# Optimization experiments

Measured on AMD Instinct MI355X. Metric: run time of the kernel, lower is better.

## Reference

```python
import jax, jax.numpy as jnp
import numpy as np

N, E, C = 8192, 8192, 256
AVG_DEG = 32


def _linear(x, w, b):
    return x @ w + b


def setup_inputs() -> dict:
    key = jax.random.key(0)
    ks = jax.random.split(key, 20)
    s = 1.0 / np.sqrt(C)
    x = jax.random.normal(ks[0], (N, C), dtype=jnp.float32)
    # binary adjacency with avg degree ~32 (unweighted COO -> dense 0/1 rep)
    adj = (jax.random.uniform(ks[1], (N, N)) < (AVG_DEG / N)).astype(jnp.float32)
    tar_ei = jax.random.randint(ks[2], (2, E), 0, N, dtype=jnp.int32)
    p = {
        'xlin_w1': jax.random.uniform(ks[3], (C, C), minval=-s, maxval=s),
        'xlin_b1': jnp.zeros((C,), jnp.float32),
        'xlin_w2': jax.random.uniform(ks[4], (C, C), minval=-s, maxval=s),
        'xlin_b2': jnp.zeros((C,), jnp.float32),
        'xcn_w1': jax.random.uniform(ks[5], (C, C), minval=-s, maxval=s),
        'xcn_b1': jnp.zeros((C,), jnp.float32),
        'xcn_w2': jax.random.uniform(ks[6], (C, C), minval=-s, maxval=s),
        'xcn_b2': jnp.zeros((C,), jnp.float32),
        'xij_w': jax.random.uniform(ks[7], (C, C), minval=-s, maxval=s),
        'xij_b': jnp.zeros((C,), jnp.float32),
        'lin_w1': jax.random.uniform(ks[8], (C, C), minval=-s, maxval=s),
        'lin_b1': jnp.zeros((C,), jnp.float32),
        'lin_w2': jax.random.uniform(ks[9], (C, 1), minval=-s, maxval=s),
        'lin_b2': jnp.zeros((1,), jnp.float32),
        'beta': jnp.ones((1,), jnp.float32),
    }
    return {'x': x, 'adj': adj, 'tar_ei': tar_ei, **p}


def reference(x, adj, tar_ei,
              xlin_w1, xlin_b1, xlin_w2, xlin_b2,
              xcn_w1, xcn_b1, xcn_w2, xcn_b2,
              xij_w, xij_b,
              lin_w1, lin_b1, lin_w2, lin_b2, beta):
    i, j = tar_ei[0], tar_ei[1]
    xi = x[i]                      # [E, C]
    xj = x[j]                      # [E, C]
    # x = x + xlin(x): Linear-ReLU-Linear-ReLU (dropout inactive, ln=Identity)
    h = x + jax.nn.relu(_linear(jax.nn.relu(_linear(x, xlin_w1, xlin_b1)), xlin_w2, xlin_b2))
    # adjoverlap: common-neighbor mask per target edge, cn[e,k] = A[i_e,k]*A[j_e,k]
    cn = adj[i] * adj[j]           # [E, N]
    # spmm_add(cn, h)
    xcn = cn @ h                   # [E, C]
    # xijlin: Linear-ReLU (tailact -> Identity tail)
    xij = jax.nn.relu(_linear(xi * xj, xij_w, xij_b))
    # xcnlin: Linear-ReLU-Linear-ReLU
    xcn = jax.nn.relu(_linear(jax.nn.relu(_linear(xcn, xcn_w1, xcn_b1)), xcn_w2, xcn_b2))
    # lin: Linear-ReLU-Linear(out)
    z = xcn * beta + xij
    out = _linear(jax.nn.relu(_linear(z, lin_w1, lin_b1)), lin_w2, lin_b2)
    return out  # [E, 1]
```

## Files before the change

### kernel.cpp

```cpp
#include <hip/hip_runtime.h>
#include <cstdint>
#include <cstddef>


#define C_DIM   256
#define N_NODES 8192
#define E_EDGES 8192

typedef short bf16x8 __attribute__((ext_vector_type(8)));
typedef float f32x4  __attribute__((ext_vector_type(4)));

struct WPtrs { const float* p[6]; };

__device__ __forceinline__ unsigned short bf16_rne(float a) {
    unsigned u = __float_as_uint(a);
    u += 0x7FFFu + ((u >> 16) & 1u);
    return (unsigned short)(u >> 16);
}
__device__ __forceinline__ void split2(float v, short& h, short& l) {
    unsigned short hb = bf16_rne(v);
    h = (short)hb;
    l = (short)bf16_rne(v - __uint_as_float((unsigned)hb << 16));
}

__global__ __launch_bounds__(256) void k_prep(const float* __restrict__ adj,
                                              unsigned long long* __restrict__ bits,
                                              WPtrs wp, short* __restrict__ WFH,
                                              short* __restrict__ WFL) {
    const int t = threadIdx.x;
    if (blockIdx.x < 48) {
        __shared__ float tile[32][257];
        const int g  = blockIdx.x >> 3;
        const int kf = blockIdx.x & 7;
        const float* W = wp.p[g];
        #pragma unroll
        for (int p = 0; p < 8; ++p) {
            int s = t + (p << 8);
            int row = s >> 6, c4 = s & 63;
            float4 v = *(const float4*)&W[(size_t)(kf * 32 + row) * C_DIM + (c4 << 2)];
            tile[row][(c4 << 2) + 0] = v.x; tile[row][(c4 << 2) + 1] = v.y;
            tile[row][(c4 << 2) + 2] = v.z; tile[row][(c4 << 2) + 3] = v.w;
        }
        __syncthreads();
        #pragma unroll
        for (int p = 0; p < 4; ++p) {
            int s = t + (p << 8);
            int nf = s >> 6, lane = s & 63;
            int q = lane >> 4, fr = lane & 15;
            short h[8], l[8];
            #pragma unroll
            for (int e = 0; e < 8; ++e)
                split2(tile[q * 8 + e][nf * 16 + fr], h[e], l[e]);
            int dst = (g << 16) + (((kf * 16 + nf) << 6) + lane) * 8;
            *(short4*)&WFH[dst]     = make_short4(h[0], h[1], h[2], h[3]);
            *(short4*)&WFH[dst + 4] = make_short4(h[4], h[5], h[6], h[7]);
            *(short4*)&WFL[dst]     = make_short4(l[0], l[1], l[2], l[3]);
            *(short4*)&WFL[dst + 4] = make_short4(l[4], l[5], l[6], l[7]);
        }
    } else {
        const int TOTALW = N_NODES * N_NODES / 64;
        const int gw   = ((int)blockIdx.x - 48) * 4 + (t >> 6);
        const int lane = t & 63;
        const int NW   = 2048 * 4;
        for (int w = gw << 3; w < TOTALW; w += NW << 3) {
            float v[8];
            #pragma unroll
            for (int r = 0; r < 8; ++r)
                v[r] = adj[((size_t)(w + r) << 6) + lane];
            unsigned long long m[8];
            #pragma unroll
            for (int r = 0; r < 8; ++r)
                m[r] = __ballot(v[r] > 0.5f);
            if (lane == 0) {
                #pragma unroll
                for (int r = 0; r < 4; ++r) {
                    ulonglong2 u2; u2.x = m[2 * r]; u2.y = m[2 * r + 1];
                    *(ulonglong2*)&bits[w + 2 * r] = u2;
                }
            }
        }
    }
}

template<int MODE>
__device__ __forceinline__ void layer_sb(
    const short (*INH)[C_DIM], const short (*INL)[C_DIM],
    const short* __restrict__ WH, const short* __restrict__ WL,
    const float* __restrict__ bias,
    short (*POH)[C_DIM], short (*POL)[C_DIM], float (*FO)[C_DIM],
    float beta, const float* __restrict__ w2, float* __restrict__ out32)
{
    const int t = threadIdx.x, lane = t & 63, wq = t >> 6;
    const int fr = lane & 15, q = lane >> 4;
    f32x4 acc[2];
    #pragma unroll
    for (int i = 0; i < 2; ++i)
        #pragma unroll
        for (int r = 0; r < 4; ++r) acc[i][r] = 0.f;

    #pragma unroll 2
    for (int kf = 0; kf < 8; ++kf) {
        bf16x8 aH[2], aL[2];
        #pragma unroll
        for (int mf = 0; mf < 2; ++mf) {
            const int row = mf * 16 + fr;
            const int cc = (((kf << 2) + q) ^ (row & 7)) << 3;
            aH[mf] = *(const bf16x8*)&INH[row][cc];
            aL[mf] = *(const bf16x8*)&INL[row][cc];
        }
        const int wo = (((kf << 4) + wq) * 64 + lane) * 8;
        bf16x8 bH = *(const bf16x8*)&WH[wo];
        bf16x8 bL = *(const bf16x8*)&WL[wo];
        #pragma unroll
        for (int mf = 0; mf < 2; ++mf) {
            acc[mf] = __builtin_amdgcn_mfma_f32_16x16x32_bf16(aH[mf], bH, acc[mf], 0, 0, 0);
            acc[mf] = __builtin_amdgcn_mfma_f32_16x16x32_bf16(aH[mf], bL, acc[mf], 0, 0, 0);
            acc[mf] = __builtin_amdgcn_mfma_f32_16x16x32_bf16(aL[mf], bH, acc[mf], 0, 0, 0);
        }
    }

    const int col = (wq << 4) + fr;
    const float bb = bias[col];
    float gs[2][4];
    if (MODE == 4) {
        #pragma unroll
        for (int mf = 0; mf < 2; ++mf)
            #pragma unroll
            for (int r = 0; r < 4; ++r) gs[mf][r] = 0.f;
    }
    const float w2c = (MODE == 4) ? w2[col] : 0.f;
    #pragma unroll
    for (int mf = 0; mf < 2; ++mf)
        #pragma unroll
        for (int r = 0; r < 4; ++r) {
            const int row = mf * 16 + q * 4 + r;
            float v = fmaxf(acc[mf][r] + bb, 0.f);
            if (MODE == 0 || MODE == 1) {
                if (MODE == 1) v = v * beta + FO[row][col];
                short h, l;
                split2(v, h, l);
                const int cw = (((col >> 3) ^ (row & 7)) << 3) + (col & 7);
                POH[row][cw] = h;
                POL[row][cw] = l;
            } else if (MODE == 2) {
                FO[row][col] = v;
            } else {
                gs[mf][r] += v * w2c;
            }
        }
    if (MODE == 4) {
        #pragma unroll
        for (int mf = 0; mf < 2; ++mf)
            #pragma unroll
            for (int r = 0; r < 4; ++r) {
                float s = gs[mf][r];
                s += __shfl_xor(s, 1); s += __shfl_xor(s, 2);
                s += __shfl_xor(s, 4); s += __shfl_xor(s, 8);
                if (fr == 0) atomicAdd(&out32[mf * 16 + q * 4 + r], s);
            }
    }
}

__device__ __forceinline__ void layer_h2(
    const short (*INH)[C_DIM], const short (*INL)[C_DIM],
    const short* __restrict__ WH, const short* __restrict__ WL,
    const float* __restrict__ bias, const int* __restrict__ inst, int nrows,
    const float* __restrict__ xsrc, float (*XCN)[C_DIM])
{
    const int t = threadIdx.x, lane = t & 63, wq = t >> 6;
    const int fr = lane & 15, q = lane >> 4;
    f32x4 acc[2];
    #pragma unroll
    for (int i = 0; i < 2; ++i)
        #pragma unroll
        for (int r = 0; r < 4; ++r) acc[i][r] = 0.f;

    #pragma unroll 2
    for (int kf = 0; kf < 8; ++kf) {
        bf16x8 aH[2], aL[2];
        #pragma unroll
        for (int mf = 0; mf < 2; ++mf) {
            const int row = mf * 16 + fr;
            const int cc = (((kf << 2) + q) ^ (row & 7)) << 3;
            aH[mf] = *(const bf16x8*)&INH[row][cc];
            aL[mf] = *(const bf16x8*)&INL[row][cc];
        }
        const int wo = (((kf << 4) + wq) * 64 + lane) * 8;
        bf16x8 bH = *(const bf16x8*)&WH[wo];
        bf16x8 bL = *(const bf16x8*)&WL[wo];
        #pragma unroll
        for (int mf = 0; mf < 2; ++mf) {
            acc[mf] = __builtin_amdgcn_mfma_f32_16x16x32_bf16(aH[mf], bH, acc[mf], 0, 0, 0);
            acc[mf] = __builtin_amdgcn_mfma_f32_16x16x32_bf16(aH[mf], bL, acc[mf], 0, 0, 0);
            acc[mf] = __builtin_amdgcn_mfma_f32_16x16x32_bf16(aL[mf], bH, acc[mf], 0, 0, 0);
        }
    }
    const int col = (wq << 4) + fr;
    const float bb = bias[col];
    #pragma unroll
    for (int mf = 0; mf < 2; ++mf)
        #pragma unroll
        for (int r = 0; r < 4; ++r) {
            const int row = mf * 16 + q * 4 + r;
            if (row < nrows) {
                const int pk = inst[row];
                const int e  = pk >> 16;
                const int k  = pk & 0xffff;
                float v = fmaxf(acc[mf][r] + bb, 0.f) + xsrc[(size_t)k * C_DIM + col];
                atomicAdd(&XCN[e][col], v);
            }
        }
}

__global__ __launch_bounds__(1024, 1) void k_edge_mega(
    const unsigned long long* __restrict__ bits, const float* __restrict__ x,
    const int* __restrict__ tar,
    const short* __restrict__ WFH, const short* __restrict__ WFL,
    const float* __restrict__ b1x, const float* __restrict__ b2x,
    const float* __restrict__ bxij, const float* __restrict__ bcn1,
    const float* __restrict__ bcn2, const float* __restrict__ blin1,
    const float* __restrict__ betap, const float* __restrict__ w2,
    const float* __restrict__ b2o, float* __restrict__ out)
{
    __shared__ short AH[32][C_DIM], AL[32][C_DIM];
    __shared__ short BH[32][C_DIM], BL[32][C_DIM];
    __shared__ float CF[32][C_DIM];
    __shared__ int   eij2[32][2];
    __shared__ int   inst[1024];
    __shared__ int   cntot;
    __shared__ float out32[32];
    const int e0 = blockIdx.x << 5;
    const int t = threadIdx.x;
    if (t < 32) {
        eij2[t][0] = tar[e0 + t];
        eij2[t][1] = tar[E_EDGES + e0 + t];
        out32[t] = 0.f;
    }
    if (t == 0) cntot = 0;
    __syncthreads();
    #pragma unroll
    for (int p = 0; p < 8; ++p) {
        int idx = (p << 10) + t;
        CF[idx >> 8][idx & 255] = 0.f;
    }
    {
        const int le = t >> 5, sub = t & 31;
        const size_t bi = (size_t)eij2[le][0] * 128;
        const size_t bj = (size_t)eij2[le][1] * 128;
        #pragma unroll
        for (int w4 = 0; w4 < 4; ++w4) {
            const int w = (sub << 2) + w4;
            unsigned long long m = bits[bi + w] & bits[bj + w];
            while (m) {
                int b = __builtin_ctzll(m);
                int slot = atomicAdd(&cntot, 1);
                if (slot < 1024) inst[slot] = (le << 16) | ((w << 6) + b);
                m &= m - 1;
            }
        }
    }
    __syncthreads();
    const int ctot = min(cntot, 1024);
    for (int c0 = 0; c0 < ctot; c0 += 32) {
        const int nrows = min(32, ctot - c0);
        #pragma unroll
        for (int p = 0; p < 8; ++p) {
            int idx = (p << 10) + t;
            int r = idx >> 8, c = idx & 255;
            float v = 0.f;
            if (r < nrows) {
                int k = inst[c0 + r] & 0xffff;
                v = x[(size_t)k * C_DIM + c];
            }
            short h, l;
            split2(v, h, l);
            int cw = (((c >> 3) ^ (r & 7)) << 3) + (c & 7);
            AH[r][cw] = h;
            AL[r][cw] = l;
        }
        __syncthreads();
        layer_sb<0>(AH, AL, WFH + 0 * 65536, WFL + 0 * 65536, b1x,
                    BH, BL, nullptr, 0.f, nullptr, nullptr);
        __syncthreads();
        layer_h2(BH, BL, WFH + 1 * 65536, WFL + 1 * 65536, b2x,
                 inst + c0, nrows, x, CF);
        __syncthreads();
    }
    #pragma unroll
    for (int p = 0; p < 8; ++p) {
        int idx = (p << 10) + t;
        int r = idx >> 8, c = idx & 255;
        short h, l;
        split2(CF[r][c], h, l);
        int cw = (((c >> 3) ^ (r & 7)) << 3) + (c & 7);
        BH[r][cw] = h;
        BL[r][cw] = l;
    }
    __syncthreads();
    #pragma unroll
    for (int p = 0; p < 8; ++p) {
        int idx = (p << 10) + t;
        int e = idx >> 8, c = idx & 255;
        float v = x[(size_t)eij2[e][0] * C_DIM + c] * x[(size_t)eij2[e][1] * C_DIM + c];
        short h, l;
        split2(v, h, l);
        int cw = (((c >> 3) ^ (e & 7)) << 3) + (c & 7);
        AH[e][cw] = h;
        AL[e][cw] = l;
    }
    __syncthreads();
    const float beta = betap[0];
    layer_sb<2>(AH, AL, WFH + 2 * 65536, WFL + 2 * 65536, bxij,
                nullptr, nullptr, CF, 0.f, nullptr, nullptr);
    __syncthreads();
    layer_sb<0>(BH, BL, WFH + 3 * 65536, WFL + 3 * 65536, bcn1,
                AH, AL, nullptr, 0.f, nullptr, nullptr);
    __syncthreads();
    layer_sb<1>(AH, AL, WFH + 4 * 65536, WFL + 4 * 65536, bcn2,
                BH, BL, CF, beta, nullptr, nullptr);
    __syncthreads();
    layer_sb<4>(BH, BL, WFH + 5 * 65536, WFL + 5 * 65536, blin1,
                nullptr, nullptr, nullptr, 0.f, w2, out32);
    __syncthreads();
    if (t < 32) out[e0 + t] = out32[t] + b2o[0];
}

extern "C" void kernel_launch(void* const* d_in, const int* in_sizes, int n_in,
                              void* d_out, int out_size, void* d_ws, size_t ws_size,
                              hipStream_t stream) {
    const float* x       = (const float*)d_in[0];
    const float* adj     = (const float*)d_in[1];
    const int*   tar_ei  = (const int*)  d_in[2];
    const float* xlin_w1 = (const float*)d_in[3];
    const float* xlin_b1 = (const float*)d_in[4];
    const float* xlin_w2 = (const float*)d_in[5];
    const float* xlin_b2 = (const float*)d_in[6];
    const float* xcn_w1  = (const float*)d_in[7];
    const float* xcn_b1  = (const float*)d_in[8];
    const float* xcn_w2  = (const float*)d_in[9];
    const float* xcn_b2  = (const float*)d_in[10];
    const float* xij_w   = (const float*)d_in[11];
    const float* xij_b   = (const float*)d_in[12];
    const float* lin_w1  = (const float*)d_in[13];
    const float* lin_b1  = (const float*)d_in[14];
    const float* lin_w2  = (const float*)d_in[15];
    const float* lin_b2  = (const float*)d_in[16];
    const float* beta    = (const float*)d_in[17];
    float* out = (float*)d_out;

    char* ws = (char*)d_ws;
    const size_t MB = 1024 * 1024;
    unsigned long long* bits = (unsigned long long*)(ws);
    short* WFH  = (short*)(ws +  8 * MB);
    short* WFL  = (short*)(ws +  9 * MB);

    WPtrs wp;
    wp.p[0] = xlin_w1; wp.p[1] = xlin_w2; wp.p[2] = xij_w;
    wp.p[3] = xcn_w1;  wp.p[4] = xcn_w2;  wp.p[5] = lin_w1;

    hipLaunchKernelGGL(k_prep, dim3(48 + 2048), dim3(256), 0, stream,
                       adj, bits, wp, WFH, WFL);
    hipLaunchKernelGGL(k_edge_mega, dim3(E_EDGES / 32), dim3(1024), 0, stream,
                       bits, x, tar_ei, WFH, WFL,
                       xlin_b1, xlin_b2, xij_b, xcn_b1, xcn_b2, lin_b1,
                       beta, lin_w2, lin_b2, out);
}
```

Baseline: 85.58 us.

## Move xij branch GEMM into prep kernel to overlap with adjacency bitpacking

The xi*xj gather and xij linear+ReLU layer are moved out of the edge megakernel into 256 extra blocks of the prep kernel. These blocks run alongside the memory-bound adjacency bit-packing and write fp32 results to a workspace buffer. The megakernel then reads them from global memory in the MODE 1 epilogue, which shortens its serial chain of layers. In exchange the prep blocks split weights to bf16 on the fly from strided global loads, and an extra 8 MB fp32 round trip through global memory is added.

```diff
diff --git a/kernel.cpp b/kernel.cpp
--- a/kernel.cpp
+++ b/kernel.cpp
@@ -24,9 +24,13 @@
 }
 
 __global__ __launch_bounds__(256) void k_prep(const float* __restrict__ adj,
+                                              const float* __restrict__ x,
+                                              const int* __restrict__ tar,
                                               unsigned long long* __restrict__ bits,
                                               WPtrs wp, short* __restrict__ WFH,
-                                              short* __restrict__ WFL) {
+                                              short* __restrict__ WFL,
+                                              const float* __restrict__ bxij,
+                                              float* __restrict__ XIJF) {
     const int t = threadIdx.x;
     if (blockIdx.x < 48) {
         __shared__ float tile[32][257];
@@ -57,9 +61,89 @@
             *(short4*)&WFL[dst]     = make_short4(l[0], l[1], l[2], l[3]);
             *(short4*)&WFL[dst + 4] = make_short4(l[4], l[5], l[6], l[7]);
         }
+    } else if (blockIdx.x < 304) {
+        __shared__ short XH[32][C_DIM], XL[32][C_DIM];
+        __shared__ int   eij2[32][2];
+        const int e0 = ((int)blockIdx.x - 48) << 5;
+        if (t < 32) {
+            eij2[t][0] = tar[e0 + t];
+            eij2[t][1] = tar[E_EDGES + e0 + t];
+        }
+        __syncthreads();
+        #pragma unroll
+        for (int p = 0; p < 4; ++p) {
+            int idx = (p << 8) + t;
+            int r = idx >> 5, c = (idx & 31) << 3;
+            float4 a0 = *(const float4*)&x[(size_t)eij2[r][0] * C_DIM + c];
+            float4 a1 = *(const float4*)&x[(size_t)eij2[r][0] * C_DIM + c + 4];
+            float4 b0 = *(const float4*)&x[(size_t)eij2[r][1] * C_DIM + c];
+            float4 b1 = *(const float4*)&x[(size_t)eij2[r][1] * C_DIM + c + 4];
+            float v[8] = {a0.x * b0.x, a0.y * b0.y, a0.z * b0.z, a0.w * b0.w,
+                          a1.x * b1.x, a1.y * b1.y, a1.z * b1.z, a1.w * b1.w};
+            short h[8], l[8];
+            #pragma unroll
+            for (int e = 0; e < 8; ++e) split2(v[e], h[e], l[e]);
+            int cw = (((c >> 3) ^ (r & 7)) << 3);
+            *(short4*)&XH[r][cw]     = make_short4(h[0], h[1], h[2], h[3]);
+            *(short4*)&XH[r][cw + 4] = make_short4(h[4], h[5], h[6], h[7]);
+            *(short4*)&XL[r][cw]     = make_short4(l[0], l[1], l[2], l[3]);
+            *(short4*)&XL[r][cw + 4] = make_short4(l[4], l[5], l[6], l[7]);
+        }
+        __syncthreads();
+        const int lane = t & 63, w = t >> 6;
+        const int fr = lane & 15, q = lane >> 4;
+        const float* Wg = wp.p[2];
+        f32x4 acc[2][4];
+        #pragma unroll
+        for (int mf = 0; mf < 2; ++mf)
+            #pragma unroll
+            for (int nfi = 0; nfi < 4; ++nfi)
+                #pragma unroll
+                for (int r = 0; r < 4; ++r) acc[mf][nfi][r] = 0.f;
+        for (int kf = 0; kf < 8; ++kf) {
+            bf16x8 aH[2], aL[2];
+            #pragma unroll
+            for (int mf = 0; mf < 2; ++mf) {
+                const int row = mf * 16 + fr;
+                const int cc = (((kf << 2) + q) ^ (row & 7)) << 3;
+                aH[mf] = *(const bf16x8*)&XH[row][cc];
+                aL[mf] = *(const bf16x8*)&XL[row][cc];
+            }
+            #pragma unroll
+            for (int nfi = 0; nfi < 4; ++nfi) {
+                const int nf = (w << 2) + nfi;
+                bf16x8 bH, bL;
+                #pragma unroll
+                for (int e = 0; e < 8; ++e) {
+                    float wv = Wg[(size_t)(kf * 32 + q * 8 + e) * C_DIM + (nf << 4) + fr];
+                    short h, l;
+                    split2(wv, h, l);
+                    bH[e] = h; bL[e] = l;
+                }
+                #pragma unroll
+                for (int mf = 0; mf < 2; ++mf) {
+                    acc[mf][nfi] = __builtin_amdgcn_mfma_f32_16x16x32_bf16(aH[mf], bH, acc[mf][nfi], 0, 0, 0);
+                    acc[mf][nfi] = __builtin_amdgcn_mfma_f32_16x16x32_bf16(aH[mf], bL, acc[mf][nfi], 0, 0, 0);
+                    acc[mf][nfi] = __builtin_amdgcn_mfma_f32_16x16x32_bf16(aL[mf], bH, acc[mf][nfi], 0, 0, 0);
+                }
+            }
+        }
+        #pragma unroll
+        for (int nfi = 0; nfi < 4; ++nfi) {
+            const int col = ((w << 2) + nfi) * 16 + fr;
+            const float bb = bxij[col];
+            #pragma unroll
+            for (int mf = 0; mf < 2; ++mf)
+                #pragma unroll
+                for (int r = 0; r < 4; ++r) {
+                    const int row = mf * 16 + q * 4 + r;
+                    XIJF[(size_t)(e0 + row) * C_DIM + col] =
+                        fmaxf(acc[mf][nfi][r] + bb, 0.f);
+                }
+        }
     } else {
         const int TOTALW = N_NODES * N_NODES / 64;
-        const int gw   = ((int)blockIdx.x - 48) * 4 + (t >> 6);
+        const int gw   = ((int)blockIdx.x - 304) * 4 + (t >> 6);
         const int lane = t & 63;
         const int NW   = 2048 * 4;
         for (int w = gw << 3; w < TOTALW; w += NW << 3) {
@@ -87,7 +171,8 @@
     const short (*INH)[C_DIM], const short (*INL)[C_DIM],
     const short* __restrict__ WH, const short* __restrict__ WL,
     const float* __restrict__ bias,
-    short (*POH)[C_DIM], short (*POL)[C_DIM], float (*FO)[C_DIM],
+    short (*POH)[C_DIM], short (*POL)[C_DIM],
+    const float* __restrict__ xijg, int e0,
     float beta, const float* __restrict__ w2, float* __restrict__ out32)
 {
     const int t = threadIdx.x, lane = t & 63, wq = t >> 6;
@@ -136,14 +221,12 @@
             const int row = mf * 16 + q * 4 + r;
             float v = fmaxf(acc[mf][r] + bb, 0.f);
             if (MODE == 0 || MODE == 1) {
-                if (MODE == 1) v = v * beta + FO[row][col];
+                if (MODE == 1) v = v * beta + xijg[(size_t)(e0 + row) * C_DIM + col];
                 short h, l;
                 split2(v, h, l);
                 const int cw = (((col >> 3) ^ (row & 7)) << 3) + (col & 7);
                 POH[row][cw] = h;
                 POL[row][cw] = l;
-            } else if (MODE == 2) {
-                FO[row][col] = v;
             } else {
                 gs[mf][r] += v * w2c;
             }
@@ -217,9 +300,9 @@
     const int* __restrict__ tar,
     const short* __restrict__ WFH, const short* __restrict__ WFL,
     const float* __restrict__ b1x, const float* __restrict__ b2x,
-    const float* __restrict__ bxij, const float* __restrict__ bcn1,
-    const float* __restrict__ bcn2, const float* __restrict__ blin1,
-    const float* __restrict__ betap, const float* __restrict__ w2,
+    const float* __restrict__ bcn1, const float* __restrict__ bcn2,
+    const float* __restrict__ blin1, const float* __restrict__ betap,
+    const float* __restrict__ xijg, const float* __restrict__ w2,
     const float* __restrict__ b2o, float* __restrict__ out)
 {
     __shared__ short AH[32][C_DIM], AL[32][C_DIM];
@@ -280,7 +363,7 @@
         }
         __syncthreads();
         layer_sb<0>(AH, AL, WFH + 0 * 65536, WFL + 0 * 65536, b1x,
-                    BH, BL, nullptr, 0.f, nullptr, nullptr);
+                    BH, BL, nullptr, 0, 0.f, nullptr, nullptr);
         __syncthreads();
         layer_h2(BH, BL, WFH + 1 * 65536, WFL + 1 * 65536, b2x,
                  inst + c0, nrows, x, CF);
@@ -297,30 +380,15 @@
         BL[r][cw] = l;
     }
     __syncthreads();
-    #pragma unroll
-    for (int p = 0; p < 8; ++p) {
-        int idx = (p << 10) + t;
-        int e = idx >> 8, c = idx & 255;
-        float v = x[(size_t)eij2[e][0] * C_DIM + c] * x[(size_t)eij2[e][1] * C_DIM + c];
-        short h, l;
-        split2(v, h, l);
-        int cw = (((c >> 3) ^ (e & 7)) << 3) + (c & 7);
-        AH[e][cw] = h;
-        AL[e][cw] = l;
-    }
-    __syncthreads();
     const float beta = betap[0];
-    layer_sb<2>(AH, AL, WFH + 2 * 65536, WFL + 2 * 65536, bxij,
-                nullptr, nullptr, CF, 0.f, nullptr, nullptr);
-    __syncthreads();
     layer_sb<0>(BH, BL, WFH + 3 * 65536, WFL + 3 * 65536, bcn1,
-                AH, AL, nullptr, 0.f, nullptr, nullptr);
+                AH, AL, nullptr, 0, 0.f, nullptr, nullptr);
     __syncthreads();
     layer_sb<1>(AH, AL, WFH + 4 * 65536, WFL + 4 * 65536, bcn2,
-                BH, BL, CF, beta, nullptr, nullptr);
+                BH, BL, xijg, e0, beta, nullptr, nullptr);
     __syncthreads();
     layer_sb<4>(BH, BL, WFH + 5 * 65536, WFL + 5 * 65536, blin1,
-                nullptr, nullptr, nullptr, 0.f, w2, out32);
+                nullptr, nullptr, nullptr, 0, 0.f, w2, out32);
     __syncthreads();
     if (t < 32) out[e0 + t] = out32[t] + b2o[0];
 }
@@ -353,15 +421,16 @@
     unsigned long long* bits = (unsigned long long*)(ws);
     short* WFH  = (short*)(ws +  8 * MB);
     short* WFL  = (short*)(ws +  9 * MB);
+    float* XIJF = (float*)(ws + 10 * MB);
 
     WPtrs wp;
     wp.p[0] = xlin_w1; wp.p[1] = xlin_w2; wp.p[2] = xij_w;
     wp.p[3] = xcn_w1;  wp.p[4] = xcn_w2;  wp.p[5] = lin_w1;
 
-    hipLaunchKernelGGL(k_prep, dim3(48 + 2048), dim3(256), 0, stream,
-                       adj, bits, wp, WFH, WFL);
+    hipLaunchKernelGGL(k_prep, dim3(48 + 256 + 2048), dim3(256), 0, stream,
+                       adj, x, tar_ei, bits, wp, WFH, WFL, xij_b, XIJF);
     hipLaunchKernelGGL(k_edge_mega, dim3(E_EDGES / 32), dim3(1024), 0, stream,
                        bits, x, tar_ei, WFH, WFL,
-                       xlin_b1, xlin_b2, xij_b, xcn_b1, xcn_b2, lin_b1,
-                       beta, lin_w2, lin_b2, out);
-}
+                       xlin_b1, xlin_b2, xcn_b1, xcn_b2, lin_b1,
+                       beta, XIJF, lin_w2, lin_b2, out);
+}
```

Result: slower. 107.5 us (+25.6%).

## Replace shared-memory xcn atomics with register accumulation and hoist xij layer

Applied to the files above, without the earlier changes.

The float CF shared buffer and its per-element LDS atomicAdd scatter are removed. The second xlin layer now writes its rows as split bf16 into shared memory, and each thread scans the chunk's instance list to accumulate its edge's 8 columns in registers. The xij product and its linear layer are moved to the start of the kernel and kept in registers, so the LDS round trip for xij and a separate staging pass go away. The cost is a serial loop over the instances of each chunk in every thread and extra live registers across the main loop. Rounding also changes because the summed values are stored as hi/lo bf16 pairs before accumulation.

```diff
diff --git a/kernel.cpp b/kernel.cpp
--- a/kernel.cpp
+++ b/kernel.cpp
@@ -21,6 +21,9 @@
     unsigned short hb = bf16_rne(v);
     h = (short)hb;
     l = (short)bf16_rne(v - __uint_as_float((unsigned)hb << 16));
+}
+__device__ __forceinline__ float bf2f(short h) {
+    return __uint_as_float(((unsigned)(unsigned short)h) << 16);
 }
 
 __global__ __launch_bounds__(256) void k_prep(const float* __restrict__ adj,
@@ -82,22 +85,17 @@
     }
 }
 
-template<int MODE>
-__device__ __forceinline__ void layer_sb(
+__device__ __forceinline__ void layer_core(
     const short (*INH)[C_DIM], const short (*INL)[C_DIM],
     const short* __restrict__ WH, const short* __restrict__ WL,
-    const float* __restrict__ bias,
-    short (*POH)[C_DIM], short (*POL)[C_DIM], float (*FO)[C_DIM],
-    float beta, const float* __restrict__ w2, float* __restrict__ out32)
+    f32x4 acc[2])
 {
     const int t = threadIdx.x, lane = t & 63, wq = t >> 6;
     const int fr = lane & 15, q = lane >> 4;
-    f32x4 acc[2];
     #pragma unroll
     for (int i = 0; i < 2; ++i)
         #pragma unroll
         for (int r = 0; r < 4; ++r) acc[i][r] = 0.f;
-
     #pragma unroll 2
     for (int kf = 0; kf < 8; ++kf) {
         bf16x8 aH[2], aL[2];
@@ -118,98 +116,6 @@
             acc[mf] = __builtin_amdgcn_mfma_f32_16x16x32_bf16(aL[mf], bH, acc[mf], 0, 0, 0);
         }
     }
-
-    const int col = (wq << 4) + fr;
-    const float bb = bias[col];
-    float gs[2][4];
-    if (MODE == 4) {
-        #pragma unroll
-        for (int mf = 0; mf < 2; ++mf)
-            #pragma unroll
-            for (int r = 0; r < 4; ++r) gs[mf][r] = 0.f;
-    }
-    const float w2c = (MODE == 4) ? w2[col] : 0.f;
-    #pragma unroll
-    for (int mf = 0; mf < 2; ++mf)
-        #pragma unroll
-        for (int r = 0; r < 4; ++r) {
-            const int row = mf * 16 + q * 4 + r;
-            float v = fmaxf(acc[mf][r] + bb, 0.f);
-            if (MODE == 0 || MODE == 1) {
-                if (MODE == 1) v = v * beta + FO[row][col];
-                short h, l;
-                split2(v, h, l);
-                const int cw = (((col >> 3) ^ (row & 7)) << 3) + (col & 7);
-                POH[row][cw] = h;
-                POL[row][cw] = l;
-            } else if (MODE == 2) {
-                FO[row][col] = v;
-            } else {
-                gs[mf][r] += v * w2c;
-            }
-        }
-    if (MODE == 4) {
-        #pragma unroll
-        for (int mf = 0; mf < 2; ++mf)
-            #pragma unroll
-            for (int r = 0; r < 4; ++r) {
-                float s = gs[mf][r];
-                s += __shfl_xor(s, 1); s += __shfl_xor(s, 2);
-                s += __shfl_xor(s, 4); s += __shfl_xor(s, 8);
-                if (fr == 0) atomicAdd(&out32[mf * 16 + q * 4 + r], s);
-            }
-    }
-}
-
-__device__ __forceinline__ void layer_h2(
-    const short (*INH)[C_DIM], const short (*INL)[C_DIM],
-    const short* __restrict__ WH, const short* __restrict__ WL,
-    const float* __restrict__ bias, const int* __restrict__ inst, int nrows,
-    const float* __restrict__ xsrc, float (*XCN)[C_DIM])
-{
-    const int t = threadIdx.x, lane = t & 63, wq = t >> 6;
-    const int fr = lane & 15, q = lane >> 4;
-    f32x4 acc[2];
-    #pragma unroll
-    for (int i = 0; i < 2; ++i)
-        #pragma unroll
-        for (int r = 0; r < 4; ++r) acc[i][r] = 0.f;
-
-    #pragma unroll 2
-    for (int kf = 0; kf < 8; ++kf) {
-        bf16x8 aH[2], aL[2];
-        #pragma unroll
-        for (int mf = 0; mf < 2; ++mf) {
-            const int row = mf * 16 + fr;
-            const int cc = (((kf << 2) + q) ^ (row & 7)) << 3;
-            aH[mf] = *(const bf16x8*)&INH[row][cc];
-            aL[mf] = *(const bf16x8*)&INL[row][cc];
-        }
-        const int wo = (((kf << 4) + wq) * 64 + lane) * 8;
-        bf16x8 bH = *(const bf16x8*)&WH[wo];
-        bf16x8 bL = *(const bf16x8*)&WL[wo];
-        #pragma unroll
-        for (int mf = 0; mf < 2; ++mf) {
-            acc[mf] = __builtin_amdgcn_mfma_f32_16x16x32_bf16(aH[mf], bH, acc[mf], 0, 0, 0);
-            acc[mf] = __builtin_amdgcn_mfma_f32_16x16x32_bf16(aH[mf], bL, acc[mf], 0, 0, 0);
-            acc[mf] = __builtin_amdgcn_mfma_f32_16x16x32_bf16(aL[mf], bH, acc[mf], 0, 0, 0);
-        }
-    }
-    const int col = (wq << 4) + fr;
-    const float bb = bias[col];
-    #pragma unroll
-    for (int mf = 0; mf < 2; ++mf)
-        #pragma unroll
-        for (int r = 0; r < 4; ++r) {
-            const int row = mf * 16 + q * 4 + r;
-            if (row < nrows) {
-                const int pk = inst[row];
-                const int e  = pk >> 16;
-                const int k  = pk & 0xffff;
-                float v = fmaxf(acc[mf][r] + bb, 0.f) + xsrc[(size_t)k * C_DIM + col];
-                atomicAdd(&XCN[e][col], v);
-            }
-        }
 }
 
 __global__ __launch_bounds__(1024, 1) void k_edge_mega(
@@ -224,13 +130,17 @@
 {
     __shared__ short AH[32][C_DIM], AL[32][C_DIM];
     __shared__ short BH[32][C_DIM], BL[32][C_DIM];
-    __shared__ float CF[32][C_DIM];
     __shared__ int   eij2[32][2];
     __shared__ int   inst[1024];
     __shared__ int   cntot;
     __shared__ float out32[32];
     const int e0 = blockIdx.x << 5;
     const int t = threadIdx.x;
+    const int lane = t & 63, wq = t >> 6;
+    const int fr = lane & 15, q = lane >> 4;
+    const int et = t >> 5;
+    const int c8 = (t & 31) << 3;
+
     if (t < 32) {
         eij2[t][0] = tar[e0 + t];
         eij2[t][1] = tar[E_EDGES + e0 + t];
@@ -238,10 +148,17 @@
     }
     if (t == 0) cntot = 0;
     __syncthreads();
+
     #pragma unroll
     for (int p = 0; p < 8; ++p) {
         int idx = (p << 10) + t;
-        CF[idx >> 8][idx & 255] = 0.f;
+        int e = idx >> 8, c = idx & 255;
+        float v = x[(size_t)eij2[e][0] * C_DIM + c] * x[(size_t)eij2[e][1] * C_DIM + c];
+        short h, l;
+        split2(v, h, l);
+        int cw = (((c >> 3) ^ (e & 7)) << 3) + (c & 7);
+        BH[e][cw] = h;
+        BL[e][cw] = l;
     }
     {
         const int le = t >> 5, sub = t & 31;
@@ -260,6 +177,23 @@
         }
     }
     __syncthreads();
+
+    float xijr[2][4];
+    {
+        f32x4 acc[2];
+        layer_core(BH, BL, WFH + 2 * 65536, WFL + 2 * 65536, acc);
+        const int col = (wq << 4) + fr;
+        const float bb = bxij[col];
+        #pragma unroll
+        for (int mf = 0; mf < 2; ++mf)
+            #pragma unroll
+            for (int r = 0; r < 4; ++r)
+                xijr[mf][r] = fmaxf(acc[mf][r] + bb, 0.f);
+    }
+
+    float xcnreg[8];
+    #pragma unroll
+    for (int u = 0; u < 8; ++u) xcnreg[u] = 0.f;
     const int ctot = min(cntot, 1024);
     for (int c0 = 0; c0 < ctot; c0 += 32) {
         const int nrows = min(32, ctot - c0);
@@ -279,48 +213,137 @@
             AL[r][cw] = l;
         }
         __syncthreads();
-        layer_sb<0>(AH, AL, WFH + 0 * 65536, WFL + 0 * 65536, b1x,
-                    BH, BL, nullptr, 0.f, nullptr, nullptr);
-        __syncthreads();
-        layer_h2(BH, BL, WFH + 1 * 65536, WFL + 1 * 65536, b2x,
-                 inst + c0, nrows, x, CF);
-        __syncthreads();
-    }
-    #pragma unroll
-    for (int p = 0; p < 8; ++p) {
-        int idx = (p << 10) + t;
-        int r = idx >> 8, c = idx & 255;
-        short h, l;
-        split2(CF[r][c], h, l);
-        int cw = (((c >> 3) ^ (r & 7)) << 3) + (c & 7);
-        BH[r][cw] = h;
-        BL[r][cw] = l;
-    }
-    __syncthreads();
-    #pragma unroll
-    for (int p = 0; p < 8; ++p) {
-        int idx = (p << 10) + t;
-        int e = idx >> 8, c = idx & 255;
-        float v = x[(size_t)eij2[e][0] * C_DIM + c] * x[(size_t)eij2[e][1] * C_DIM + c];
-        short h, l;
-        split2(v, h, l);
-        int cw = (((c >> 3) ^ (e & 7)) << 3) + (c & 7);
-        AH[e][cw] = h;
-        AL[e][cw] = l;
-    }
-    __syncthreads();
+        {
+            f32x4 acc[2];
+            layer_core(AH, AL, WFH + 0 * 65536, WFL + 0 * 65536, acc);
+            const int col = (wq << 4) + fr;
+            const float bb = b1x[col];
+            #pragma unroll
+            for (int mf = 0; mf < 2; ++mf)
+                #pragma unroll
+                for (int r = 0; r < 4; ++r) {
+                    const int row = mf * 16 + q * 4 + r;
+                    float v = fmaxf(acc[mf][r] + bb, 0.f);
+                    short h, l;
+                    split2(v, h, l);
+                    const int cw = (((col >> 3) ^ (row & 7)) << 3) + (col & 7);
+                    BH[row][cw] = h;
+                    BL[row][cw] = l;
+                }
+        }
+        __syncthreads();
+        {
+            f32x4 acc[2];
+            layer_core(BH, BL, WFH + 1 * 65536, WFL + 1 * 65536, acc);
+            const int col = (wq << 4) + fr;
+            const float bb = b2x[col];
+            #pragma unroll
+            for (int mf = 0; mf < 2; ++mf)
+                #pragma unroll
+                for (int r = 0; r < 4; ++r) {
+                    const int row = mf * 16 + q * 4 + r;
+                    if (row < nrows) {
+                        const int k = inst[c0 + row] & 0xffff;
+                        float v = fmaxf(acc[mf][r] + bb, 0.f) +
+                                  x[(size_t)k * C_DIM + col];
+                        short h, l;
+                        split2(v, h, l);
+                        const int cw = (((col >> 3) ^ (row & 7)) << 3) + (col & 7);
+                        AH[row][cw] = h;
+                        AL[row][cw] = l;
+                    }
+                }
+        }
+        __syncthreads();
+        for (int s = 0; s < nrows; ++s) {
+            int pk = inst[c0 + s];
+            if ((pk >> 16) == et) {
+                const int cw = ((c8 >> 3) ^ (s & 7)) << 3;
+                short4 h0 = *(const short4*)&AH[s][cw];
+                short4 h1 = *(const short4*)&AH[s][cw + 4];
+                short4 l0 = *(const short4*)&AL[s][cw];
+                short4 l1 = *(const short4*)&AL[s][cw + 4];
+                xcnreg[0] += bf2f(h0.x) + bf2f(l0.x);
+                xcnreg[1] += bf2f(h0.y) + bf2f(l0.y);
+                xcnreg[2] += bf2f(h0.z) + bf2f(l0.z);
+                xcnreg[3] += bf2f(h0.w) + bf2f(l0.w);
+                xcnreg[4] += bf2f(h1.x) + bf2f(l1.x);
+                xcnreg[5] += bf2f(h1.y) + bf2f(l1.y);
+                xcnreg[6] += bf2f(h1.z) + bf2f(l1.z);
+                xcnreg[7] += bf2f(h1.w) + bf2f(l1.w);
+            }
+        }
+        __syncthreads();
+    }
+
+    {
+        const int cwb = ((c8 >> 3) ^ (et & 7)) << 3;
+        short h[8], l[8];
+        #pragma unroll
+        for (int u = 0; u < 8; ++u) split2(xcnreg[u], h[u], l[u]);
+        *(short4*)&AH[et][cwb]     = make_short4(h[0], h[1], h[2], h[3]);
+        *(short4*)&AH[et][cwb + 4] = make_short4(h[4], h[5], h[6], h[7]);
+        *(short4*)&AL[et][cwb]     = make_short4(l[0], l[1], l[2], l[3]);
+        *(short4*)&AL[et][cwb + 4] = make_short4(l[4], l[5], l[6], l[7]);
+    }
+    __syncthreads();
+
     const float beta = betap[0];
-    layer_sb<2>(AH, AL, WFH + 2 * 65536, WFL + 2 * 65536, bxij,
-                nullptr, nullptr, CF, 0.f, nullptr, nullptr);
-    __syncthreads();
-    layer_sb<0>(BH, BL, WFH + 3 * 65536, WFL + 3 * 65536, bcn1,
-                AH, AL, nullptr, 0.f, nullptr, nullptr);
-    __syncthreads();
-    layer_sb<1>(AH, AL, WFH + 4 * 65536, WFL + 4 * 65536, bcn2,
-                BH, BL, CF, beta, nullptr, nullptr);
-    __syncthreads();
-    layer_sb<4>(BH, BL, WFH + 5 * 65536, WFL + 5 * 65536, blin1,
-                nullptr, nullptr, nullptr, 0.f, w2, out32);
+    {
+        f32x4 acc[2];
+        layer_core(AH, AL, WFH + 3 * 65536, WFL + 3 * 65536, acc);
+        const int col = (wq << 4) + fr;
+        const float bb = bcn1[col];
+        #pragma unroll
+        for (int mf = 0; mf < 2; ++mf)
+            #pragma unroll
+            for (int r = 0; r < 4; ++r) {
+                const int row = mf * 16 + q * 4 + r;
+                float v = fmaxf(acc[mf][r] + bb, 0.f);
+                short h, l;
+                split2(v, h, l);
+                const int cw = (((col >> 3) ^ (row & 7)) << 3) + (col & 7);
+                BH[row][cw] = h;
+                BL[row][cw] = l;
+            }
+    }
+    __syncthreads();
+    {
+        f32x4 acc[2];
+        layer_core(BH, BL, WFH + 4 * 65536, WFL + 4 * 65536, acc);
+        const int col = (wq << 4) + fr;
+        const float bb = bcn2[col];
+        #pragma unroll
+        for (int mf = 0; mf < 2; ++mf)
+            #pragma unroll
+            for (int r = 0; r < 4; ++r) {
+                const int row = mf * 16 + q * 4 + r;
+                float v = fmaxf(acc[mf][r] + bb, 0.f) * beta + xijr[mf][r];
+                short h, l;
+                split2(v, h, l);
+                const int cw = (((col >> 3) ^ (row & 7)) << 3) + (col & 7);
+                AH[row][cw] = h;
+                AL[row][cw] = l;
+            }
+    }
+    __syncthreads();
+    {
+        f32x4 acc[2];
+        layer_core(AH, AL, WFH + 5 * 65536, WFL + 5 * 65536, acc);
+        const int col = (wq << 4) + fr;
+        const float bb = blin1[col];
+        const float w2c = w2[col];
+        #pragma unroll
+        for (int mf = 0; mf < 2; ++mf) {
+            #pragma unroll
+            for (int r = 0; r < 4; ++r) {
+                float s = fmaxf(acc[mf][r] + bb, 0.f) * w2c;
+                s += __shfl_xor(s, 1); s += __shfl_xor(s, 2);
+                s += __shfl_xor(s, 4); s += __shfl_xor(s, 8);
+                if (fr == 0) atomicAdd(&out32[mf * 16 + q * 4 + r], s);
+            }
+        }
+    }
     __syncthreads();
     if (t < 32) out[e0 + t] = out32[t] + b2o[0];
 }
```

New measurement: 80.72 us. 1.06x faster.
